# Optimization experiments

Measured on AMD Instinct MI355X. Metric: run time of the kernel, lower is better.

Reference implementation:

```python
import jax, jax.numpy as jnp
import numpy as np

B, T, D_IN = 16, 4096, 512
D_EMB, N_CODES = 256, 1024


def setup_inputs() -> dict:
    key = jax.random.key(0)
    k1, k2, k3, k4 = jax.random.split(key, 4)
    z = jax.random.normal(k1, (B, T, D_IN), dtype=jnp.float32)
    embedding = jax.random.normal(k2, (N_CODES, D_EMB), dtype=jnp.float32)
    # torch Linear weight layout [out_features, in_features], bias=False
    proj_down_w = jax.random.normal(k3, (D_EMB, D_IN), dtype=jnp.float32) * (1.0 / np.sqrt(D_IN))
    proj_up_w = jax.random.normal(k4, (D_IN, D_EMB), dtype=jnp.float32) * (1.0 / np.sqrt(D_EMB))
    return {"z": z, "embedding": embedding, "proj_down_w": proj_down_w, "proj_up_w": proj_up_w}


def _quantize_to_code(z_e, codebook):
    # z_e: [b, t, d]; codebook: [n, d] -> indices [b, t]
    b, t, d = z_e.shape
    z_flat = z_e.reshape(b * t, d)
    dist = (jnp.sum(z_flat * z_flat, axis=1, keepdims=True)
            - 2.0 * (z_flat @ codebook.T)
            + jnp.sum(codebook * codebook, axis=1)[None, :])  # [(b t), n]
    return jnp.argmin(dist, axis=1).reshape(b, t)


def reference(z, embedding, proj_down_w, proj_up_w):
    # proj_down: z @ W_down^T
    z_e = jnp.einsum('btd,ed->bte', z, proj_down_w)  # [b, t, D_EMB]
    code = _quantize_to_code(z_e, embedding)
    z_q = embedding[code]  # gather: [b, t, D_EMB]
    diff2 = (z_q - z_e) ** 2
    commitment_loss = diff2.mean(axis=(1, 2))  # [b]
    codebook_loss = diff2.mean(axis=(1, 2))    # [b] (same values fwd; differ in grad)
    # straight-through estimator (training mode)
    z_q_st = z_e + jax.lax.stop_gradient(z_q - z_e)
    z_q_out = jnp.einsum('bte,de->btd', z_q_st, proj_up_w)  # [b, t, D_IN]
    return (z_q_out, commitment_loss, codebook_loss, code, z_e)
```

## Files before the change

kernel.cpp:

```cpp
#include <hip/hip_runtime.h>
#include <stdint.h>

#define DIN  512
#define DE   256
#define NC   1024
#define M_   65536
#define FLAGCAP 16384

typedef unsigned short u16;
typedef __attribute__((ext_vector_type(8))) short short8_t;
typedef __attribute__((ext_vector_type(4))) float f32x4_t;
typedef __attribute__((ext_vector_type(16))) float f32x16_t;

__device__ __forceinline__ float bf2f(u16 u) {
    unsigned x = ((unsigned)u) << 16; return __builtin_bit_cast(float, x);
}
__device__ __forceinline__ u16 f2bf(float f) {
    unsigned x = __builtin_bit_cast(unsigned, f);
    x += 0x7fffu + ((x >> 16) & 1u);
    return (u16)(x >> 16);
}
__device__ __forceinline__ void cvt8_hl(float4 a, float4 b, short8_t& h, short8_t& l) {
    float v[8] = {a.x,a.y,a.z,a.w, b.x,b.y,b.z,b.w};
#pragma unroll
    for (int j = 0; j < 8; ++j) {
        u16 hh = f2bf(v[j]);
        h[j] = (short)hh; l[j] = (short)f2bf(v[j] - bf2f(hh));
    }
}
__device__ __forceinline__ short8_t cvt8(float4 a, float4 b) {
    float v[8] = {a.x,a.y,a.z,a.w, b.x,b.y,b.z,b.w};
    short8_t h;
#pragma unroll
    for (int j = 0; j < 8; ++j) h[j] = (short)f2bf(v[j]);
    return h;
}

__global__ void k_init(const float* __restrict__ emb, const float* __restrict__ Wd,
                       u16* __restrict__ embH, u16* __restrict__ embL,
                       u16* __restrict__ WdH,  u16* __restrict__ WdL,
                       float* __restrict__ cnorm,
                       float* __restrict__ lossacc, int* __restrict__ flagcnt) {
    int tid = blockIdx.x * 256 + threadIdx.x;
    for (int i = tid; i < DE * DIN; i += 65536) {
        float v = Wd[i]; u16 h = f2bf(v);
        WdH[i] = h; WdL[i] = f2bf(v - bf2f(h));
    }
    for (int i = tid; i < NC * DE; i += 65536) {
        float v = emb[i]; u16 h = f2bf(v);
        embH[i] = h; embL[i] = f2bf(v - bf2f(h));
    }
    if (tid < NC) {
        const float* c = emb + (size_t)tid * DE;
        double s = 0.0;
        for (int j = 0; j < DE; ++j) { double v = c[j]; s += v * v; }
        cnorm[tid] = (float)s;
    }
    if (tid < 16) lossacc[tid] = 0.f;
    if (tid == 16) *flagcnt = 0;
}

__global__ __launch_bounds__(256, 1) void k_pup(
        const float* __restrict__ emb, const float* __restrict__ Wu,
        float* __restrict__ P) {
    __shared__ __align__(16) float le[64][260];
    __shared__ __align__(16) float lw[64][260];
    const int bi = blockIdx.x >> 3, bj = blockIdx.x & 7;
    const int t = threadIdx.x;
    {
        const int r = t >> 2, q = (t & 3) * 64;
        const float* se = emb + (size_t)(bi * 64 + r) * DE + q;
        const float* sw = Wu  + (size_t)(bj * 64 + r) * DE + q;
#pragma unroll
        for (int i = 0; i < 16; ++i) {
            *(float4*)&le[r][q + i * 4] = *(const float4*)(se + i * 4);
            *(float4*)&lw[r][q + i * 4] = *(const float4*)(sw + i * 4);
        }
    }
    __syncthreads();
    const int ci = (t >> 4) * 4, oi = (t & 15) * 4;
    float acc[4][4];
#pragma unroll
    for (int a = 0; a < 4; ++a)
#pragma unroll
        for (int b = 0; b < 4; ++b) acc[a][b] = 0.f;
    for (int k = 0; k < DE; k += 4) {
        float4 av[4], bv[4];
#pragma unroll
        for (int a = 0; a < 4; ++a) av[a] = *(const float4*)&le[ci + a][k];
#pragma unroll
        for (int b = 0; b < 4; ++b) bv[b] = *(const float4*)&lw[oi + b][k];
#pragma unroll
        for (int a = 0; a < 4; ++a)
#pragma unroll
            for (int b = 0; b < 4; ++b)
                acc[a][b] += av[a].x * bv[b].x + av[a].y * bv[b].y
                           + av[a].z * bv[b].z + av[a].w * bv[b].w;
    }
#pragma unroll
    for (int a = 0; a < 4; ++a)
#pragma unroll
        for (int b = 0; b < 4; ++b)
            P[(size_t)(bi * 64 + ci + a) * DIN + bj * 64 + oi + b] = acc[a][b];
}

__global__ __launch_bounds__(256, 2) void k_fz(
        const float* __restrict__ Z,
        const u16* __restrict__ WdH, const u16* __restrict__ WdL,
        const u16* __restrict__ embH, const u16* __restrict__ embL,
        const float* __restrict__ cnorm,
        float* __restrict__ zeF,
        u16* __restrict__ codew, float* __restrict__ out_codef,
        int* __restrict__ flaglist,
        int* __restrict__ flagcnt, float* __restrict__ lossacc) {
    __shared__ __align__(16) u16 aH[2][128 * 40];
    __shared__ __align__(16) u16 aL[2][128 * 40];
    __shared__ float lCn[NC];
    __shared__ float lLoss[128];
    const int m0 = blockIdx.x * 128;
    const int t = threadIdx.x, lane = t & 63, wv = t >> 6;
    const int lc = lane & 31, hi = lane >> 5;
    const int zrow = m0 + wv * 32 + lc;
    const int zsr = t >> 1, zss = (t & 1) * 16;

    for (int i = t; i < NC; i += 256) lCn[i] = cnorm[i];

#define Z_LD(kt_) { \
        const float4* p = (const float4*)(Z + (size_t)(m0 + zsr) * DIN + (kt_) * 32 + zss); \
        zf[0] = p[0]; zf[1] = p[1]; zf[2] = p[2]; zf[3] = p[3]; }
#define Z_WR(b_) { \
        short8_t h0, l0, h1, l1; \
        cvt8_hl(zf[0], zf[1], h0, l0); cvt8_hl(zf[2], zf[3], h1, l1); \
        *(short8_t*)&aH[b_][zsr * 40 + zss]     = h0; \
        *(short8_t*)&aH[b_][zsr * 40 + zss + 8] = h1; \
        *(short8_t*)&aL[b_][zsr * 40 + zss]     = l0; \
        *(short8_t*)&aL[b_][zsr * 40 + zss + 8] = l1; }
#define WD_LD(kt_, H_, L_) { \
        H_[0] = *(const short8_t*)(WdHr + (kt_) * 32 + hi * 8); \
        H_[1] = *(const short8_t*)(WdHr + (kt_) * 32 + 16 + hi * 8); \
        L_[0] = *(const short8_t*)(WdLr + (kt_) * 32 + hi * 8); \
        L_[1] = *(const short8_t*)(WdLr + (kt_) * 32 + 16 + hi * 8); }

    for (int mh = 0; mh < 2; ++mh) {
        const int nb = mh * 128;
        const int wdrow = nb + wv * 32 + lc;
        const u16* WdHr = WdH + (size_t)wdrow * DIN;
        const u16* WdLr = WdL + (size_t)wdrow * DIN;

        float4 zf[4];
        short8_t wh[2], wl[2], nwh[2], nwl[2];
        Z_LD(0);
        WD_LD(0, wh, wl);
        __syncthreads();
        Z_WR(0);
        __syncthreads();

        f32x16_t acc[4];
#pragma unroll
        for (int s = 0; s < 4; ++s)
#pragma unroll
            for (int r = 0; r < 16; ++r) acc[s][r] = 0.f;

        for (int kt = 0; kt < 16; ++kt) {
            if (kt < 15) { Z_LD(kt + 1); WD_LD(kt + 1, nwh, nwl); }
            const int buf = kt & 1;
#pragma unroll
            for (int ks = 0; ks < 2; ++ks) {
#pragma unroll
                for (int s = 0; s < 4; ++s) {
                    const int lo = (s * 32 + lc) * 40 + ks * 16 + hi * 8;
                    short8_t zh = *(const short8_t*)&aH[buf][lo];
                    short8_t zl = *(const short8_t*)&aL[buf][lo];
                    acc[s] = __builtin_amdgcn_mfma_f32_32x32x16_bf16(zh, wh[ks], acc[s], 0, 0, 0);
                    acc[s] = __builtin_amdgcn_mfma_f32_32x32x16_bf16(zh, wl[ks], acc[s], 0, 0, 0);
                    acc[s] = __builtin_amdgcn_mfma_f32_32x32x16_bf16(zl, wh[ks], acc[s], 0, 0, 0);
                }
            }
            if (kt < 15) {
                __syncthreads();
                Z_WR((kt + 1) & 1);
                zf[0] = zf[0];
                wh[0] = nwh[0]; wh[1] = nwh[1];
                wl[0] = nwl[0]; wl[1] = nwl[1];
                __syncthreads();
            }
        }
#pragma unroll
        for (int s = 0; s < 4; ++s)
#pragma unroll
            for (int r = 0; r < 16; ++r) {
                const int zr = m0 + s * 32 + (r & 3) + 8 * (r >> 2) + 4 * hi;
                zeF[(size_t)zr * DE + nb + wv * 32 + lc] = acc[s][r];
            }
    }
#undef Z_LD
#undef Z_WR
#undef WD_LD
    __syncthreads();

    short8_t bh[16], bl[16];
    float rn = 0.f;
#pragma unroll
    for (int c = 0; c < 16; ++c) {
        const float4* zp = (const float4*)(zeF + (size_t)zrow * DE + c * 16 + hi * 8);
        float4 a = zp[0], b = zp[1];
        rn += a.x*a.x + a.y*a.y + a.z*a.z + a.w*a.w
            + b.x*b.x + b.y*b.y + b.z*b.z + b.w*b.w;
        cvt8_hl(a, b, bh[c], bl[c]);
    }
    rn += __shfl_xor(rn, 32, 64);

#define STAGE_E(ct_, kt_, b_) { \
        _Pragma("unroll") \
        for (int j = 0; j < 2; ++j) { \
            int idx = t + j * 256; \
            int row = idx >> 2, seg = (idx & 3) * 8; \
            size_t off = (size_t)((ct_) * 128 + row) * DE + (kt_) * 32 + seg; \
            uint4 vh = *(const uint4*)(embH + off); \
            uint4 vl = *(const uint4*)(embL + off); \
            *(uint4*)&aH[b_][row * 40 + seg] = vh; \
            *(uint4*)&aL[b_][row * 40 + seg] = vl; \
        } }

    float best = 3.4e38f, sec = 3.4e38f; int bidx = 0;
    STAGE_E(0, 0, 0);
    for (int ct = 0; ct < 8; ++ct) {
        f32x16_t acc[4];
#pragma unroll
        for (int s = 0; s < 4; ++s)
#pragma unroll
            for (int r = 0; r < 16; ++r) acc[s][r] = 0.f;
#pragma unroll
        for (int kt = 0; kt < 8; ++kt) {
            __syncthreads();
            if (kt < 7)      STAGE_E(ct, kt + 1, (kt + 1) & 1)
            else if (ct < 7) STAGE_E(ct + 1, 0, 0)
            const int buf = kt & 1;
#pragma unroll
            for (int ks = 0; ks < 2; ++ks) {
                const int c = kt * 2 + ks;
#pragma unroll
                for (int s = 0; s < 4; ++s) {
                    short8_t ah = *(const short8_t*)&aH[buf][(s * 32 + lc) * 40 + ks * 16 + hi * 8];
                    short8_t al = *(const short8_t*)&aL[buf][(s * 32 + lc) * 40 + ks * 16 + hi * 8];
                    acc[s] = __builtin_amdgcn_mfma_f32_32x32x16_bf16(ah, bh[c], acc[s], 0, 0, 0);
                    acc[s] = __builtin_amdgcn_mfma_f32_32x32x16_bf16(ah, bl[c], acc[s], 0, 0, 0);
                    acc[s] = __builtin_amdgcn_mfma_f32_32x32x16_bf16(al, bh[c], acc[s], 0, 0, 0);
                }
            }
        }
#pragma unroll
        for (int s = 0; s < 4; ++s)
#pragma unroll
            for (int r = 0; r < 16; ++r) {
                const int cidx = ct * 128 + s * 32 + (r & 3) + 8 * (r >> 2) + 4 * hi;
                float d = fmaf(-2.f, acc[s][r], lCn[cidx]);
                bool lt = d < best;
                sec  = lt ? best : fminf(sec, d);
                best = lt ? d : best;
                bidx = lt ? cidx : bidx;
            }
    }
#undef STAGE_E
    {
        float ob = __shfl_xor(best, 32, 64);
        float os = __shfl_xor(sec,  32, 64);
        int   oi = __shfl_xor(bidx, 32, 64);
        float ns = fminf(fminf(sec, os), fmaxf(best, ob));
        if (ob < best) { best = ob; bidx = oi; }
        sec = ns;
    }
    if (lane < 32) {
        codew[zrow] = (u16)bidx;
        out_codef[zrow] = (float)bidx;
        if (sec - best < 0.02f) {
            int pos = atomicAdd(flagcnt, 1);
            if (pos < FLAGCAP) flaglist[pos] = zrow;
        }
        lLoss[wv * 32 + lc] = rn + best;
    }
    __syncthreads();
    for (int str = 64; str > 0; str >>= 1) {
        if (t < str) lLoss[t] += lLoss[t + str];
        __syncthreads();
    }
    if (t == 0) atomicAdd(&lossacc[m0 >> 12], lLoss[0]);
}

__global__ __launch_bounds__(256) void k_refine(
        const float* __restrict__ Z, const float* __restrict__ Wd,
        const float* __restrict__ emb,
        const int* __restrict__ flaglist, const int* __restrict__ flagcnt,
        u16* __restrict__ codew, float* __restrict__ out_codef) {
    __shared__ float  lz[DIN];
    __shared__ double lze[DE];
    __shared__ double ld[256];
    __shared__ int    li[256];
    int n = *flagcnt; if (n < 0) n = 0; if (n > FLAGCAP) n = FLAGCAP;
    int t = threadIdx.x;
    for (int f = blockIdx.x; f < n; f += gridDim.x) {
        int row = flaglist[f] & (M_ - 1);
        __syncthreads();
        for (int i = t; i < DIN; i += 256) lz[i] = Z[(size_t)row * DIN + i];
        __syncthreads();
        double a = 0.0;
        const float* wr = Wd + (size_t)t * DIN;
        for (int k = 0; k < DIN; ++k) a += (double)lz[k] * (double)wr[k];
        lze[t] = a;
        __syncthreads();
        double bd = 1e300; int bi = 0;
        for (int cc = 0; cc < 4; ++cc) {
            int c = cc * 256 + t;
            const float* cr = emb + (size_t)c * DE;
            double s = 0.0;
            for (int e = 0; e < DE; ++e) {
                double diff = lze[e] - (double)cr[e];
                s += diff * diff;
            }
            if (s < bd) { bd = s; bi = c; }
        }
        ld[t] = bd; li[t] = bi;
        __syncthreads();
        for (int str = 128; str > 0; str >>= 1) {
            if (t < str) {
                double od = ld[t + str]; int oi = li[t + str];
                if (od < ld[t] || (od == ld[t] && oi < li[t])) { ld[t] = od; li[t] = oi; }
            }
            __syncthreads();
        }
        if (t == 0) { codew[row] = (u16)li[0]; out_codef[row] = (float)li[0]; }
        __syncthreads();
    }
}

__global__ void k_loss(const float* __restrict__ lossacc,
                       float* __restrict__ out_commit, float* __restrict__ out_codebook) {
    int tid = threadIdx.x;
    if (tid < 16) {
        float v = lossacc[tid] * (1.f / 1048576.f);
        out_commit[tid] = v; out_codebook[tid] = v;
    }
}

__global__ __launch_bounds__(256) void k_gather(
        const float* __restrict__ P, const float* __restrict__ out_code,
        float* __restrict__ out) {
    const int g = blockIdx.x * 256 + threadIdx.x;
    const float4* P4 = (const float4*)P;
    float4* O4 = (float4*)out;
    for (int u = g; u < M_ * 128; u += 524288) {
        const int row = u >> 7, seg = u & 127;
        const int c = (int)out_code[row] & (NC - 1);
        O4[(size_t)row * 128 + seg] = P4[(size_t)c * 128 + seg];
    }
}

__global__ __launch_bounds__(512) void k_gemm3(
        const float* __restrict__ emb, const float* __restrict__ Wu,
        const float* __restrict__ out_code, float* __restrict__ out) {
    __shared__ __align__(16) u16 gA[128 * 264];
    const int bz = blockIdx.x >> 1, nh = blockIdx.x & 1;
    const int m0 = bz * 128;
    const int t = threadIdx.x, lane = t & 63, wv = t >> 6;
    const int lr = lane & 15, lg = lane >> 4;
    {
        const int row = t >> 2, seg = (t & 3) * 64;
        const int code = (int)out_code[m0 + row] & (NC - 1);
        const float* src = emb + (size_t)code * DE + seg;
#pragma unroll
        for (int j = 0; j < 8; ++j) {
            const float4* p = (const float4*)(src + j * 8);
            *(short8_t*)&gA[row * 264 + seg + j * 8] = cvt8(p[0], p[1]);
        }
    }
    __syncthreads();

    const int nbase = nh * 256 + wv * 32;
    f32x4_t acc[8][2];
#pragma unroll
    for (int i = 0; i < 8; ++i)
#pragma unroll
        for (int j = 0; j < 2; ++j) acc[i][j] = (f32x4_t){0.f, 0.f, 0.f, 0.f};

#pragma unroll
    for (int kt = 0; kt < 8; ++kt) {
        const int k0 = kt * 32 + lg * 8;
        short8_t b0, b1;
        {
            const float4* p = (const float4*)(Wu + (size_t)(nbase + lr) * DE + k0);
            b0 = cvt8(p[0], p[1]);
            const float4* q = (const float4*)(Wu + (size_t)(nbase + 16 + lr) * DE + k0);
            b1 = cvt8(q[0], q[1]);
        }
#pragma unroll
        for (int mi = 0; mi < 8; ++mi) {
            short8_t a = *(const short8_t*)&gA[(mi * 16 + lr) * 264 + k0];
            acc[mi][0] = __builtin_amdgcn_mfma_f32_16x16x32_bf16(a, b0, acc[mi][0], 0, 0, 0);
            acc[mi][1] = __builtin_amdgcn_mfma_f32_16x16x32_bf16(a, b1, acc[mi][1], 0, 0, 0);
        }
    }
#pragma unroll
    for (int mi = 0; mi < 8; ++mi)
#pragma unroll
        for (int reg = 0; reg < 4; ++reg) {
            const int zr = m0 + mi * 16 + lg * 4 + reg;
            out[(size_t)zr * DIN + nbase + lr]      = acc[mi][0][reg];
            out[(size_t)zr * DIN + nbase + 16 + lr] = acc[mi][1][reg];
        }
}

extern "C" void kernel_launch(void* const* d_in, const int* in_sizes, int n_in,
                              void* d_out, int out_size, void* d_ws, size_t ws_size,
                              hipStream_t stream) {
    const float* Z   = (const float*)d_in[0];
    const float* E   = (const float*)d_in[1];
    const float* Wd  = (const float*)d_in[2];
    const float* Wu  = (const float*)d_in[3];

    float* out       = (float*)d_out;
    float* out_zq    = out;
    float* out_com   = out + 33554432;
    float* out_cb    = out + 33554448;
    float* out_code  = out + 33554464;
    float* out_ze    = out + 33620000;

    char* scr = (char*)d_out;
    u16*   embH     = (u16*)  (scr + 0);
    u16*   embL     = (u16*)  (scr + 524288);
    u16*   WdH      = (u16*)  (scr + 1048576);
    u16*   WdL      = (u16*)  (scr + 1310720);
    float* cnorm    = (float*)(scr + 1572864);
    u16*   codew    = (u16*)  (scr + 1839104);
    int*   flaglist = (int*)  (scr + 1970176);
    int*   flagcnt  = (int*)  (scr + 2035712);
    float* lossacc  = (float*)(scr + 2035776);
    (void)in_sizes; (void)n_in; (void)out_size;

    const bool useP = (ws_size >= (size_t)NC * DIN * sizeof(float));
    float* P = (float*)d_ws;

    k_init  <<<256,  256, 0, stream>>>(E, Wd, embH, embL, WdH, WdL, cnorm,
                                       lossacc, flagcnt);
    if (useP)
        k_pup <<<128, 256, 0, stream>>>(E, Wu, P);
    k_fz    <<<512,  256, 0, stream>>>(Z, WdH, WdL, embH, embL, cnorm, out_ze,
                                       codew, out_code, flaglist, flagcnt, lossacc);
    k_refine<<<128,  256, 0, stream>>>(Z, Wd, E, flaglist, flagcnt, codew, out_code);
    k_loss  <<<1,    64,  0, stream>>>(lossacc, out_com, out_cb);
    if (useP)
        k_gather<<<2048, 256, 0, stream>>>(P, out_code, out_zq);
    else
        k_gemm3 <<<1024, 512, 0, stream>>>(E, Wu, out_code, out_zq);
}
```

Baseline: 338.6 us.

## Stage codebook tiles via direct global-to-LDS loads with XOR swizzle; fold loss kernel

Codebook tiles in the distance GEMM are now copied straight from global memory into LDS with global_load_lds 16-byte transfers, instead of passing through registers. An XOR swizzle on the 8-element groups, with a 32-element row stride in place of the padded 40, is meant to avoid LDS bank conflicts on the MFMA operand reads. The tiny loss-finalize kernel is merged into the refine kernel to save one launch. The direct LDS loads rely on the existing barriers for completion ordering, which may be fragile, and the swizzle has to match exactly between the writes and the reads.

```diff
diff --git a/kernel.cpp b/kernel.cpp
--- a/kernel.cpp
+++ b/kernel.cpp
@@ -34,6 +34,12 @@
 #pragma unroll
     for (int j = 0; j < 8; ++j) h[j] = (short)f2bf(v[j]);
     return h;
+}
+
+__device__ __forceinline__ void gl_lds16(const u16* g, u16* l) {
+    __builtin_amdgcn_global_load_lds(
+        (const __attribute__((address_space(1))) unsigned int*)g,
+        (__attribute__((address_space(3))) unsigned int*)l, 16, 0, 0);
 }
 
 __global__ void k_init(const float* __restrict__ emb, const float* __restrict__ Wd,
@@ -179,7 +185,6 @@
             if (kt < 15) {
                 __syncthreads();
                 Z_WR((kt + 1) & 1);
-                zf[0] = zf[0];
                 wh[0] = nwh[0]; wh[1] = nwh[1];
                 wl[0] = nwl[0]; wl[1] = nwl[1];
                 __syncthreads();
@@ -210,20 +215,24 @@
     }
     rn += __shfl_xor(rn, 32, 64);
 
-#define STAGE_E(ct_, kt_, b_) { \
+#define STAGE_GL(ct_, kt_) { \
         _Pragma("unroll") \
         for (int j = 0; j < 2; ++j) { \
-            int idx = t + j * 256; \
-            int row = idx >> 2, seg = (idx & 3) * 8; \
-            size_t off = (size_t)((ct_) * 128 + row) * DE + (kt_) * 32 + seg; \
-            uint4 vh = *(const uint4*)(embH + off); \
-            uint4 vl = *(const uint4*)(embL + off); \
-            *(uint4*)&aH[b_][row * 40 + seg] = vh; \
-            *(uint4*)&aL[b_][row * 40 + seg] = vl; \
+            int p = t + j * 256; \
+            int row = p >> 2, gp = p & 3; \
+            int gl = gp ^ ((row >> 1) & 3); \
+            size_t off = (size_t)((ct_) * 128 + row) * DE + (kt_) * 32 + gl * 8; \
+            gl_lds16(embH + off, &aH[bufn][p * 8]); \
+            gl_lds16(embL + off, &aL[bufn][p * 8]); \
         } }
 
+    const int rho = (lc >> 1) & 3;
+
     float best = 3.4e38f, sec = 3.4e38f; int bidx = 0;
-    STAGE_E(0, 0, 0);
+    {
+        const int bufn = 0;
+        STAGE_GL(0, 0);
+    }
     for (int ct = 0; ct < 8; ++ct) {
         f32x16_t acc[4];
 #pragma unroll
@@ -233,16 +242,20 @@
 #pragma unroll
         for (int kt = 0; kt < 8; ++kt) {
             __syncthreads();
-            if (kt < 7)      STAGE_E(ct, kt + 1, (kt + 1) & 1)
-            else if (ct < 7) STAGE_E(ct + 1, 0, 0)
+            {
+                const int bufn = (kt + 1) & 1;
+                if (kt < 7)      STAGE_GL(ct, kt + 1)
+                else if (ct < 7) STAGE_GL(ct + 1, 0)
+            }
             const int buf = kt & 1;
 #pragma unroll
             for (int ks = 0; ks < 2; ++ks) {
                 const int c = kt * 2 + ks;
 #pragma unroll
                 for (int s = 0; s < 4; ++s) {
-                    short8_t ah = *(const short8_t*)&aH[buf][(s * 32 + lc) * 40 + ks * 16 + hi * 8];
-                    short8_t al = *(const short8_t*)&aL[buf][(s * 32 + lc) * 40 + ks * 16 + hi * 8];
+                    const int lo = (s * 32 + lc) * 32 + (((ks * 2 + hi) ^ rho) << 3);
+                    short8_t ah = *(const short8_t*)&aH[buf][lo];
+                    short8_t al = *(const short8_t*)&aL[buf][lo];
                     acc[s] = __builtin_amdgcn_mfma_f32_32x32x16_bf16(ah, bh[c], acc[s], 0, 0, 0);
                     acc[s] = __builtin_amdgcn_mfma_f32_32x32x16_bf16(ah, bl[c], acc[s], 0, 0, 0);
                     acc[s] = __builtin_amdgcn_mfma_f32_32x32x16_bf16(al, bh[c], acc[s], 0, 0, 0);
@@ -261,7 +274,7 @@
                 bidx = lt ? cidx : bidx;
             }
     }
-#undef STAGE_E
+#undef STAGE_GL
     {
         float ob = __shfl_xor(best, 32, 64);
         float os = __shfl_xor(sec,  32, 64);
@@ -291,13 +304,19 @@
         const float* __restrict__ Z, const float* __restrict__ Wd,
         const float* __restrict__ emb,
         const int* __restrict__ flaglist, const int* __restrict__ flagcnt,
-        u16* __restrict__ codew, float* __restrict__ out_codef) {
+        u16* __restrict__ codew, float* __restrict__ out_codef,
+        const float* __restrict__ lossacc,
+        float* __restrict__ out_commit, float* __restrict__ out_codebook) {
     __shared__ float  lz[DIN];
     __shared__ double lze[DE];
     __shared__ double ld[256];
     __shared__ int    li[256];
+    int t = threadIdx.x;
+    if (blockIdx.x == 0 && t < 16) {
+        float v = lossacc[t] * (1.f / 1048576.f);
+        out_commit[t] = v; out_codebook[t] = v;
+    }
     int n = *flagcnt; if (n < 0) n = 0; if (n > FLAGCAP) n = FLAGCAP;
-    int t = threadIdx.x;
     for (int f = blockIdx.x; f < n; f += gridDim.x) {
         int row = flaglist[f] & (M_ - 1);
         __syncthreads();
@@ -330,15 +349,6 @@
         }
         if (t == 0) { codew[row] = (u16)li[0]; out_codef[row] = (float)li[0]; }
         __syncthreads();
-    }
-}
-
-__global__ void k_loss(const float* __restrict__ lossacc,
-                       float* __restrict__ out_commit, float* __restrict__ out_codebook) {
-    int tid = threadIdx.x;
-    if (tid < 16) {
-        float v = lossacc[tid] * (1.f / 1048576.f);
-        out_commit[tid] = v; out_codebook[tid] = v;
     }
 }
 
@@ -445,8 +455,8 @@
         k_pup <<<128, 256, 0, stream>>>(E, Wu, P);
     k_fz    <<<512,  256, 0, stream>>>(Z, WdH, WdL, embH, embL, cnorm, out_ze,
                                        codew, out_code, flaglist, flagcnt, lossacc);
-    k_refine<<<128,  256, 0, stream>>>(Z, Wd, E, flaglist, flagcnt, codew, out_code);
-    k_loss  <<<1,    64,  0, stream>>>(lossacc, out_com, out_cb);
+    k_refine<<<128,  256, 0, stream>>>(Z, Wd, E, flaglist, flagcnt, codew, out_code,
+                                       lossacc, out_com, out_cb);
     if (useP)
         k_gather<<<2048, 256, 0, stream>>>(P, out_code, out_zq);
     else
```

Measured after the change: 336.5 us. About the same (-0.6%).
